# Optimization experiments

Measured on AMD Instinct MI355X. Metric: run time of the kernel, lower is better.

Reference implementation:

```python
import jax, jax.numpy as jnp
import numpy as np

N = 50000      # nodes
E = 800000     # edges (before self-loops)
IN = 512       # in_dim
HID = 128      # hidden_dim
HEADS = 4
NEG_SLOPE = 0.2


def setup_inputs() -> dict:
    key = jax.random.key(0)
    ks = jax.random.split(key, 20)
    s = 0.05
    inp = {
        'x': jax.random.normal(ks[0], (N, IN), jnp.float32),
        'edge_index': jax.random.randint(ks[1], (2, E), 0, N, dtype=jnp.int32),
        # layer 0: GATConv(IN -> HID, heads=HEADS)
        'W0': jax.random.normal(ks[2], (HEADS * HID, IN), jnp.float32) * s,
        'a_src0': jax.random.normal(ks[3], (HEADS, HID), jnp.float32) * s,
        'a_dst0': jax.random.normal(ks[4], (HEADS, HID), jnp.float32) * s,
        'b0': jnp.zeros((HEADS * HID,), jnp.float32),
        # layer 1: GATConv(HEADS*HID -> HID, heads=HEADS)
        'W1': jax.random.normal(ks[5], (HEADS * HID, HEADS * HID), jnp.float32) * s,
        'a_src1': jax.random.normal(ks[6], (HEADS, HID), jnp.float32) * s,
        'a_dst1': jax.random.normal(ks[7], (HEADS, HID), jnp.float32) * s,
        'b1': jnp.zeros((HEADS * HID,), jnp.float32),
        # layer 2: GATConv(HEADS*HID -> HID, heads=1)
        'W2': jax.random.normal(ks[8], (HID, HEADS * HID), jnp.float32) * s,
        'a_src2': jax.random.normal(ks[9], (1, HID), jnp.float32) * s,
        'a_dst2': jax.random.normal(ks[10], (1, HID), jnp.float32) * s,
        'b2': jnp.zeros((HID,), jnp.float32),
        # output heads
        'Wv': jax.random.normal(ks[11], (HID, HID), jnp.float32) * s,
        'bv': jnp.zeros((HID,), jnp.float32),
        'Wt': jax.random.normal(ks[12], (HID, HID), jnp.float32) * s,
        'bt': jnp.zeros((HID,), jnp.float32),
    }
    return inp


def _gat_conv(x, src, dst, W, a_src, a_dst, bias, heads, n_nodes):
    """PyG-style GATConv (eval mode, att_dropout=0, self-loops pre-added)."""
    ch = a_src.shape[-1]
    h = (x @ W.T).reshape(n_nodes, heads, ch)            # [N,H,C]
    alpha_s = jnp.einsum('nhc,hc->nh', h, a_src)          # [N,H]
    alpha_d = jnp.einsum('nhc,hc->nh', h, a_dst)          # [N,H]
    e = alpha_s[src] + alpha_d[dst]                       # [E,H]
    e = jnp.where(e > 0, e, NEG_SLOPE * e)                # leaky_relu(0.2)
    # segment softmax over destination nodes
    m = jax.ops.segment_max(e, dst, num_segments=n_nodes)  # [N,H]
    e = jnp.exp(e - m[dst])
    z = jax.ops.segment_sum(e, dst, num_segments=n_nodes)  # [N,H]
    alpha = e / (z[dst] + 1e-16)                          # [E,H]
    msg = h[src] * alpha[:, :, None]                      # [E,H,C]
    out = jax.ops.segment_sum(msg, dst, num_segments=n_nodes)  # [N,H,C]
    return out.reshape(n_nodes, heads * ch) + bias


def reference(x, edge_index, W0, a_src0, a_dst0, b0, W1, a_src1, a_dst1, b1,
              W2, a_src2, a_dst2, b2, Wv, bv, Wt, bt):
    n = x.shape[0]
    loops = jnp.arange(n, dtype=edge_index.dtype)
    src = jnp.concatenate([edge_index[0], loops])
    dst = jnp.concatenate([edge_index[1], loops])

    h = _gat_conv(x, src, dst, W0, a_src0, a_dst0, b0, HEADS, n)
    h = jax.nn.relu(h)                                    # dropout is no-op in eval
    h = _gat_conv(h, src, dst, W1, a_src1, a_dst1, b1, HEADS, n)
    h = jax.nn.relu(h)
    h = _gat_conv(h, src, dst, W2, a_src2, a_dst2, b2, 1, n)  # [N,HID]

    x_vision = jax.nn.relu(h @ Wv.T + bv)
    x_text = jax.nn.relu(h @ Wt.T + bt)
    return (h, x_vision, x_text)
```

## Files before the change

kernel.cpp:

```cpp
#include <hip/hip_runtime.h>
#include <hip/hip_bf16.h>
#include <math.h>

typedef __bf16 bf16;
typedef __bf16 bf16x2 __attribute__((ext_vector_type(2)));
typedef __bf16 bf16x4 __attribute__((ext_vector_type(4)));
typedef __bf16 bf16x8 __attribute__((ext_vector_type(8)));
typedef float f32x4 __attribute__((ext_vector_type(4)));

#define NNODES 50000
#define NEDGES 800000

static __device__ __forceinline__ void gld_lds16(const void* g, void* l) {
    __builtin_amdgcn_global_load_lds((__attribute__((address_space(1))) void*)g,
                                     (__attribute__((address_space(3))) void*)l,
                                     16, 0, 0);
}

__global__ void detect_kernel(const unsigned int* __restrict__ xw, int* __restrict__ flag)
{
    const int l = threadIdx.x;
    int c = 0;
    for (int i = l; i < 4096; i += 64) {
        const unsigned int b1 = (xw[i] >> 8) & 0x7Fu;
        c += (b1 >= 0x34u && b1 <= 0x43u) ? 1 : 0;
    }
#pragma unroll
    for (int off = 32; off; off >>= 1) c += __shfl_xor(c, off);
    if (l == 0) *flag = (c < 2048) ? 1 : 0;
}

__global__ __launch_bounds__(256) void zero_out_kernel(void* out, long n, const int* __restrict__ flag)
{
    const int fp32 = *flag;
    const long i = (long)blockIdx.x * 256 + threadIdx.x;
    if (i < n) {
        if (fp32) ((float*)out)[i] = 0.f;
        else ((bf16*)out)[i] = (bf16)0.f;
    }
}

__global__ __launch_bounds__(256) void convert4_kernel(
    const void* __restrict__ in, bf16* __restrict__ out, int n4, const int* __restrict__ flag)
{
    const int fp32 = *flag;
    const int i = blockIdx.x * 256 + threadIdx.x;
    if (i >= n4) return;
    bf16x4 o;
    if (fp32) {
        const float4 v = ((const float4*)in)[i];
        o[0] = (bf16)v.x; o[1] = (bf16)v.y; o[2] = (bf16)v.z; o[3] = (bf16)v.w;
    } else {
        o = ((const bf16x4*)in)[i];
    }
    ((bf16x4*)out)[i] = o;
}

struct CvtBatch { const void* in[16]; bf16* out[16]; int n4[16]; };

__global__ __launch_bounds__(256) void convert_batch_kernel(CvtBatch b, const int* __restrict__ flag)
{
    const int fp32 = *flag;
    const int it = blockIdx.y;
    const int n4 = b.n4[it];
    const void* in = b.in[it];
    bf16* out = b.out[it];
    for (int i = blockIdx.x * 256 + threadIdx.x; i < n4; i += gridDim.x * 256) {
        bf16x4 o;
        if (fp32) {
            const float4 v = ((const float4*)in)[i];
            o[0] = (bf16)v.x; o[1] = (bf16)v.y; o[2] = (bf16)v.z; o[3] = (bf16)v.w;
        } else {
            o = ((const bf16x4*)in)[i];
        }
        ((bf16x4*)out)[i] = o;
    }
}

__global__ __launch_bounds__(256) void gemm_bt(
    const bf16* __restrict__ A, const bf16* __restrict__ B,
    bf16* __restrict__ C, int M, int N, int K,
    const bf16* __restrict__ av, const bf16* __restrict__ dv,
    float* __restrict__ aS, float* __restrict__ aD, int H)
{
    __shared__ __align__(16) bf16 As[128 * 32];
    __shared__ __align__(16) bf16 Bs[128 * 32];
    __shared__ float sPS[128];
    __shared__ float sPD[128];
    const int tid  = threadIdx.x;
    const int lane = tid & 63;
    const int w    = tid >> 6;
    const int wm   = (w >> 1) * 64, wn = (w & 1) * 64;
    const int mBase = blockIdx.y * 128, nBase = blockIdx.x * 128;
    const int hb = nBase >> 7;

    f32x4 acc[4][4];
#pragma unroll
    for (int i = 0; i < 4; i++)
#pragma unroll
        for (int j = 0; j < 4; j++)
#pragma unroll
            for (int r = 0; r < 4; r++) acc[i][j][r] = 0.f;

    const int rA   = tid >> 2;
    const int kseg = (tid & 3) * 8;
    int ra0 = mBase + rA;       if (ra0 > M - 1) ra0 = M - 1;
    int ra1 = mBase + rA + 64;  if (ra1 > M - 1) ra1 = M - 1;
    const bf16* gA0 = A + (long)ra0 * K + kseg;
    const bf16* gA1 = A + (long)ra1 * K + kseg;
    const bf16* gB0 = B + (long)(nBase + rA) * K + kseg;
    const bf16* gB1 = B + (long)(nBase + rA + 64) * K + kseg;
    bf16* lA0 = &As[tid * 8];
    bf16* lA1 = &As[(tid + 256) * 8];
    bf16* lB0 = &Bs[tid * 8];
    bf16* lB1 = &Bs[(tid + 256) * 8];

    const int quad = lane >> 4, l16 = lane & 15;

    if (tid < 128) { sPS[tid] = 0.f; sPD[tid] = 0.f; }

    for (int k0 = 0; k0 < K; k0 += 32) {
        gld_lds16(gA0 + k0, lA0);
        gld_lds16(gA1 + k0, lA1);
        gld_lds16(gB0 + k0, lB0);
        gld_lds16(gB1 + k0, lB1);
        __syncthreads();
        bf16x8 af[4], bfr[4];
#pragma unroll
        for (int i = 0; i < 4; i++) {
            af[i]  = *(const bf16x8*)&As[(wm + i * 16 + l16) * 32 + quad * 8];
            bfr[i] = *(const bf16x8*)&Bs[(wn + i * 16 + l16) * 32 + quad * 8];
        }
#pragma unroll
        for (int i = 0; i < 4; i++)
#pragma unroll
            for (int j = 0; j < 4; j++)
                acc[i][j] = __builtin_amdgcn_mfma_f32_16x16x32_bf16(af[i], bfr[j], acc[i][j], 0, 0, 0);
        __syncthreads();
    }

    float aval[4], dval[4];
#pragma unroll
    for (int j = 0; j < 4; j++) {
        const int cg = nBase + wn + j * 16 + l16;
        aval[j] = (float)av[cg];
        dval[j] = (float)dv[cg];
    }
#pragma unroll
    for (int i = 0; i < 4; i++) {
#pragma unroll
        for (int r = 0; r < 4; r++) {
            float ps = 0.f, pd = 0.f;
#pragma unroll
            for (int j = 0; j < 4; j++) {
                ps += acc[i][j][r] * aval[j];
                pd += acc[i][j][r] * dval[j];
            }
#pragma unroll
            for (int off = 8; off; off >>= 1) {
                ps += __shfl_xor(ps, off);
                pd += __shfl_xor(pd, off);
            }
            if (l16 == 0) {
                const int rl = wm + i * 16 + quad * 4 + r;
                atomicAdd(&sPS[rl], ps);
                atomicAdd(&sPD[rl], pd);
            }
        }
    }

#pragma unroll
    for (int i = 0; i < 4; i++) {
        const int row0 = mBase + wm + i * 16 + quad * 4;
#pragma unroll
        for (int j = 0; j < 4; j++) {
            const int colg = nBase + wn + j * 16 + l16;
#pragma unroll
            for (int r = 0; r < 4; r++) {
                const int row = row0 + r;
                if (row < M) C[(long)row * N + colg] = (bf16)acc[i][j][r];
            }
        }
    }

    __syncthreads();
    if (tid < 128) {
        const int row = mBase + tid;
        if (row < M) {
            aS[(long)row * H + hb] = sPS[tid];
            aD[(long)row * H + hb] = sPD[tid];
        }
    }
}

__global__ void hist_kernel(const int* __restrict__ dst, int* __restrict__ cnt, int E)
{
    const int e = blockIdx.x * blockDim.x + threadIdx.x;
    if (e < E) atomicAdd(&cnt[dst[e]], 1);
}

__global__ __launch_bounds__(256) void scan1_kernel(
    const int* __restrict__ cnt, int* __restrict__ rowptr, int* __restrict__ blksum, int n)
{
    __shared__ int buf[256];
    const int b = blockIdx.x, t = threadIdx.x, i = b * 256 + t;
    const int v = (i < n) ? cnt[i] : 0;
    buf[t] = v;
    __syncthreads();
    for (int off = 1; off < 256; off <<= 1) {
        const int add = (t >= off) ? buf[t - off] : 0;
        __syncthreads();
        buf[t] += add;
        __syncthreads();
    }
    if (i < n) rowptr[i + 1] = buf[t];
    if (t == 255) blksum[b] = buf[255];
    if (b == 0 && t == 0) rowptr[0] = 0;
}

__global__ __launch_bounds__(256) void scan2_kernel(int* __restrict__ blksum, int nb)
{
    __shared__ int buf[256];
    const int t = threadIdx.x;
    const int v = (t < nb) ? blksum[t] : 0;
    buf[t] = v;
    __syncthreads();
    for (int off = 1; off < 256; off <<= 1) {
        const int add = (t >= off) ? buf[t - off] : 0;
        __syncthreads();
        buf[t] += add;
        __syncthreads();
    }
    if (t < nb) blksum[t] = buf[t] - v;
}

__global__ __launch_bounds__(256) void scan3_kernel(
    int* __restrict__ rowptr, const int* __restrict__ blksum, int n)
{
    const int b = blockIdx.x, i = b * 256 + threadIdx.x;
    if (i < n) rowptr[i + 1] += blksum[b];
}

__global__ void fill_kernel(const int* __restrict__ src, const int* __restrict__ dst,
                            const int* __restrict__ rowptr, int* __restrict__ off,
                            int* __restrict__ col, int E)
{
    const int e = blockIdx.x * blockDim.x + threadIdx.x;
    if (e < E) {
        const int d = dst[e];
        const int p = rowptr[d] + atomicAdd(&off[d], 1);
        col[p] = src[e];
    }
}

__global__ __launch_bounds__(256) void agg4s_kernel(
    const bf16* __restrict__ h, const float* __restrict__ asrc,
    const float* __restrict__ adst, const int* __restrict__ rowptr,
    const int* __restrict__ col, const bf16* __restrict__ bias,
    bf16* __restrict__ out, int NB)
{
    __shared__ int2 ew_s[4][64];
    const int w = threadIdx.x >> 6, lane = threadIdx.x & 63;
    const int g = lane >> 4, li = lane & 15;
    const int s = blockIdx.x / NB;
    const int n = (blockIdx.x % NB) * 4 + w;
    const float ad = adst[(long)n * 4 + s];
    const int start = rowptr[n];
    const int deg   = rowptr[n + 1] - start;
    const int total = deg + 1;

    float z = 0.f;
    float acc[8];
#pragma unroll
    for (int c = 0; c < 8; c++) acc[c] = 0.f;
    const char* hbp = (const char*)h;
    const int sOff = s * 256 + li * 16;
    const int2* ews = ew_s[w];

    for (int base = 0; base < total; base += 64) {
        const int i = base + lane;
        const bool valid = i < total;
        const int sv = (i < deg) ? col[start + i] : n;
        float e = asrc[(long)sv * 4 + s] + ad;
        e = (e > 0.f) ? e : 0.2f * e;
        e = fminf(fmaxf(e, -60.f), 60.f);
        const float wv = valid ? __expf(e) : 0.f;
        ew_s[w][lane] = make_int2(sv << 10, __float_as_int(wv));
        __builtin_amdgcn_wave_barrier();
        const int cnt = min(64, total - base);
        int j = 0;
        for (; j + 16 <= cnt; j += 16) {
            const int2 v0 = ews[j + g];
            const int2 v1 = ews[j + 4 + g];
            const int2 v2 = ews[j + 8 + g];
            const int2 v3 = ews[j + 12 + g];
            const bf16x8 h0 = *(const bf16x8*)(hbp + (v0.x + sOff));
            const bf16x8 h1 = *(const bf16x8*)(hbp + (v1.x + sOff));
            const bf16x8 h2 = *(const bf16x8*)(hbp + (v2.x + sOff));
            const bf16x8 h3 = *(const bf16x8*)(hbp + (v3.x + sOff));
            const float w0 = __int_as_float(v0.y), w1 = __int_as_float(v1.y);
            const float w2 = __int_as_float(v2.y), w3 = __int_as_float(v3.y);
            z += w0 + w1 + w2 + w3;
#pragma unroll
            for (int c = 0; c < 8; c++) {
                acc[c] += w0 * (float)h0[c];
                acc[c] += w1 * (float)h1[c];
                acc[c] += w2 * (float)h2[c];
                acc[c] += w3 * (float)h3[c];
            }
        }
        for (; j < cnt; j += 4) {
            const int2 v = ews[j + g];
            const float ww = __int_as_float(v.y);
            z += ww;
            const bf16x8 hv = *(const bf16x8*)(hbp + (v.x + sOff));
#pragma unroll
            for (int c = 0; c < 8; c++) acc[c] += ww * (float)hv[c];
        }
        __builtin_amdgcn_wave_barrier();
    }

#pragma unroll
    for (int c = 0; c < 8; c++) {
        acc[c] += __shfl_xor(acc[c], 16);
        acc[c] += __shfl_xor(acc[c], 32);
    }
    z += __shfl_xor(z, 16);
    z += __shfl_xor(z, 32);

    if (g == 0) {
        const float rz = 1.f / (z + 1e-16f);
        const bf16x8 b8 = *(const bf16x8*)(bias + s * 128 + li * 8);
        bf16x8 ov;
#pragma unroll
        for (int c = 0; c < 8; c++)
            ov[c] = (bf16)fmaxf(acc[c] * rz + (float)b8[c], 0.f);
        *(bf16x8*)(out + (long)n * 512 + s * 128 + li * 8) = ov;
    }
}

__global__ __launch_bounds__(256) void agg1g_kernel(
    const bf16* __restrict__ h, const float* __restrict__ asrc,
    const float* __restrict__ adst, const int* __restrict__ rowptr,
    const int* __restrict__ col, const bf16* __restrict__ bias,
    void* __restrict__ outv, const int* __restrict__ dflag)
{
    __shared__ int2 ew_s[4][64];
    const int w = threadIdx.x >> 6, lane = threadIdx.x & 63;
    const int g = lane >> 4, li = lane & 15;
    const int n = blockIdx.x * 4 + w;
    if (n >= NNODES) return;
    const int fp32out = *dflag;
    const float ad = adst[n];
    const int start = rowptr[n];
    const int deg   = rowptr[n + 1] - start;
    const int total = deg + 1;

    float z = 0.f;
    float acc[8];
#pragma unroll
    for (int c = 0; c < 8; c++) acc[c] = 0.f;
    const char* hbp = (const char*)h;
    const int sOff = li * 16;
    const int2* ews = ew_s[w];

    for (int base = 0; base < total; base += 64) {
        const int i = base + lane;
        const bool valid = i < total;
        const int sv = (i < deg) ? col[start + i] : n;
        float e = asrc[sv] + ad;
        e = (e > 0.f) ? e : 0.2f * e;
        e = fminf(fmaxf(e, -60.f), 60.f);
        const float wv = valid ? __expf(e) : 0.f;
        ew_s[w][lane] = make_int2(sv << 8, __float_as_int(wv));
        __builtin_amdgcn_wave_barrier();
        const int cnt = min(64, total - base);
        int j = 0;
        for (; j + 16 <= cnt; j += 16) {
            const int2 v0 = ews[j + g];
            const int2 v1 = ews[j + 4 + g];
            const int2 v2 = ews[j + 8 + g];
            const int2 v3 = ews[j + 12 + g];
            const bf16x8 h0 = *(const bf16x8*)(hbp + (v0.x + sOff));
            const bf16x8 h1 = *(const bf16x8*)(hbp + (v1.x + sOff));
            const bf16x8 h2 = *(const bf16x8*)(hbp + (v2.x + sOff));
            const bf16x8 h3 = *(const bf16x8*)(hbp + (v3.x + sOff));
            const float w0 = __int_as_float(v0.y), w1 = __int_as_float(v1.y);
            const float w2 = __int_as_float(v2.y), w3 = __int_as_float(v3.y);
            z += w0 + w1 + w2 + w3;
#pragma unroll
            for (int c = 0; c < 8; c++) {
                acc[c] += w0 * (float)h0[c];
                acc[c] += w1 * (float)h1[c];
                acc[c] += w2 * (float)h2[c];
                acc[c] += w3 * (float)h3[c];
            }
        }
        for (; j < cnt; j += 4) {
            const int2 v = ews[j + g];
            const float ww = __int_as_float(v.y);
            z += ww;
            const bf16x8 hv = *(const bf16x8*)(hbp + (v.x + sOff));
#pragma unroll
            for (int c = 0; c < 8; c++) acc[c] += ww * (float)hv[c];
        }
        __builtin_amdgcn_wave_barrier();
    }

#pragma unroll
    for (int c = 0; c < 8; c++) {
        acc[c] += __shfl_xor(acc[c], 16);
        acc[c] += __shfl_xor(acc[c], 32);
    }
    z += __shfl_xor(z, 16);
    z += __shfl_xor(z, 32);

    if (g == 0) {
        const float rz = 1.f / (z + 1e-16f);
        float o[8];
#pragma unroll
        for (int c = 0; c < 8; c++)
            o[c] = acc[c] * rz + (float)bias[li * 8 + c];
        if (fp32out) {
            float* op = (float*)outv + (long)n * 128 + li * 8;
            f32x4 o0, o1;
#pragma unroll
            for (int c = 0; c < 4; c++) { o0[c] = o[c]; o1[c] = o[c + 4]; }
            *(f32x4*)op = o0;
            *(f32x4*)(op + 4) = o1;
        } else {
            bf16x8 ov;
#pragma unroll
            for (int c = 0; c < 8; c++) ov[c] = (bf16)o[c];
            *(bf16x8*)((bf16*)outv + (long)n * 128 + li * 8) = ov;
        }
    }
}

__global__ __launch_bounds__(256) void heads_kernel(
    const void* __restrict__ hbase, void* __restrict__ outv,
    const bf16* __restrict__ Wv, const bf16* __restrict__ bv,
    const bf16* __restrict__ Wt, const bf16* __restrict__ bt,
    const int* __restrict__ dflag, int N)
{
    const int fp32 = *dflag;
    __shared__ float hbuf[32][128];
    const int n0 = blockIdx.x * 32, t = threadIdx.x;
    for (int i = t; i < 32 * 128; i += 256) {
        const int node = n0 + (i >> 7), c = i & 127;
        float v = 0.f;
        if (node < N)
            v = fp32 ? ((const float*)hbase)[(long)node * 128 + c]
                     : (float)((const bf16*)hbase)[(long)node * 128 + c];
        hbuf[i >> 7][c] = v;
    }
    __syncthreads();
    const int m = t & 127;
    const bool vis = t < 128;
    const bf16* W = vis ? Wv : Wt;
    const float b = (float)(vis ? bv[m] : bt[m]);
    float acc[32];
#pragma unroll
    for (int i = 0; i < 32; i++) acc[i] = 0.f;
    for (int k0 = 0; k0 < 128; k0 += 8) {
        const bf16x8 wv8 = *(const bf16x8*)&W[m * 128 + k0];
#pragma unroll
        for (int kk = 0; kk < 8; kk++) {
            const float wk = (float)wv8[kk];
#pragma unroll
            for (int i = 0; i < 32; i++) acc[i] += hbuf[i][k0 + kk] * wk;
        }
    }
    const long sec = vis ? (long)N * 128 : (long)2 * N * 128;
#pragma unroll
    for (int i = 0; i < 32; i++) {
        const int node = n0 + i;
        if (node < N) {
            float o = fmaxf(acc[i] + b, 0.f);
            const long idx = sec + (long)node * 128 + m;
            if (fp32) ((float*)outv)[idx] = o;
            else ((bf16*)outv)[idx] = (bf16)o;
        }
    }
}

extern "C" void kernel_launch(void* const* d_in, const int* in_sizes, int n_in,
                              void* d_out, int out_size, void* d_ws, size_t ws_size,
                              hipStream_t stream)
{
    const int N = NNODES, E = NEDGES;
    const int* srcp = (const int*)d_in[1];
    const int* dstp = srcp + E;

    char* p0 = (char*)d_ws;
    char* p = p0;
    auto bump = [&](size_t b) { char* r = p; p += (b + 255) & ~(size_t)255; return r; };
    int*   dflag  = (int*)bump(256);
    bf16*  xc     = (bf16*)bump((size_t)N * 512 * 2);
    bf16*  W0c    = (bf16*)bump(262144 * 2);
    bf16*  as0c   = (bf16*)bump(512 * 2);
    bf16*  ad0c   = (bf16*)bump(512 * 2);
    bf16*  b0c    = (bf16*)bump(512 * 2);
    bf16*  W1c    = (bf16*)bump(262144 * 2);
    bf16*  as1c   = (bf16*)bump(512 * 2);
    bf16*  ad1c   = (bf16*)bump(512 * 2);
    bf16*  b1c    = (bf16*)bump(512 * 2);
    bf16*  W2c    = (bf16*)bump(65536 * 2);
    bf16*  as2c   = (bf16*)bump(128 * 2);
    bf16*  ad2c   = (bf16*)bump(128 * 2);
    bf16*  b2c    = (bf16*)bump(128 * 2);
    bf16*  Wvc    = (bf16*)bump(16384 * 2);
    bf16*  bvc    = (bf16*)bump(128 * 2);
    bf16*  Wtc    = (bf16*)bump(16384 * 2);
    bf16*  btc    = (bf16*)bump(128 * 2);
    int*   cnt    = (int*)bump((size_t)N * 4);
    int*   offs   = (int*)bump((size_t)N * 4);
    int*   rowptr = (int*)bump((size_t)(N + 1) * 4);
    int*   blksum = (int*)bump(256 * 4);
    int*   colarr = (int*)bump((size_t)E * 4);
    float* alphaS = (float*)bump((size_t)N * 4 * 4);
    float* alphaD = (float*)bump((size_t)N * 4 * 4);
    bf16*  bufA   = (bf16*)bump((size_t)N * 512 * 2);
    bf16*  bufB   = (bf16*)bump((size_t)N * 512 * 2);
    const size_t need = (size_t)(p - p0);

    detect_kernel<<<1, 64, 0, stream>>>((const unsigned int*)d_in[0], dflag);

    if (need > ws_size) {
        zero_out_kernel<<<((long)out_size + 255) / 256, 256, 0, stream>>>(d_out, out_size, dflag);
        return;
    }

    convert4_kernel<<<(N * 512 / 4 + 255) / 256, 256, 0, stream>>>(d_in[0], xc, N * 512 / 4, dflag);
    CvtBatch cb;
    const void* ins[16] = {d_in[2], d_in[3], d_in[4], d_in[5], d_in[6], d_in[7], d_in[8], d_in[9],
                           d_in[10], d_in[11], d_in[12], d_in[13], d_in[14], d_in[15], d_in[16], d_in[17]};
    bf16* outs[16] = {W0c, as0c, ad0c, b0c, W1c, as1c, ad1c, b1c,
                      W2c, as2c, ad2c, b2c, Wvc, bvc, Wtc, btc};
    const int ns4[16] = {65536, 128, 128, 128, 65536, 128, 128, 128,
                         16384, 32, 32, 32, 4096, 32, 4096, 32};
    for (int i = 0; i < 16; i++) { cb.in[i] = ins[i]; cb.out[i] = outs[i]; cb.n4[i] = ns4[i]; }
    convert_batch_kernel<<<dim3(64, 16), 256, 0, stream>>>(cb, dflag);

    const int nb = (N + 255) / 256;
    hipMemsetAsync(cnt, 0, (size_t)N * 4, stream);
    hipMemsetAsync(offs, 0, (size_t)N * 4, stream);
    hist_kernel<<<(E + 255) / 256, 256, 0, stream>>>(dstp, cnt, E);
    scan1_kernel<<<nb, 256, 0, stream>>>(cnt, rowptr, blksum, N);
    scan2_kernel<<<1, 256, 0, stream>>>(blksum, nb);
    scan3_kernel<<<nb, 256, 0, stream>>>(rowptr, blksum, N);
    fill_kernel<<<(E + 255) / 256, 256, 0, stream>>>(srcp, dstp, rowptr, offs, colarr, E);

    const int NB = N / 4;

    dim3 g0(4, (N + 127) / 128);
    gemm_bt<<<g0, 256, 0, stream>>>(xc, W0c, bufA, N, 512, 512,
                                    as0c, ad0c, alphaS, alphaD, 4);
    agg4s_kernel<<<NB * 4, 256, 0, stream>>>(bufA, alphaS, alphaD, rowptr, colarr, b0c, bufB, NB);

    gemm_bt<<<g0, 256, 0, stream>>>(bufB, W1c, bufA, N, 512, 512,
                                    as1c, ad1c, alphaS, alphaD, 4);
    agg4s_kernel<<<NB * 4, 256, 0, stream>>>(bufA, alphaS, alphaD, rowptr, colarr, b1c, bufB, NB);

    dim3 g2(1, (N + 127) / 128);
    gemm_bt<<<g2, 256, 0, stream>>>(bufB, W2c, bufA, N, 128, 512,
                                    as2c, ad2c, alphaS, alphaD, 1);
    agg1g_kernel<<<(N + 3) / 4, 256, 0, stream>>>(bufA, alphaS, alphaD, rowptr, colarr, b2c, d_out, dflag);

    heads_kernel<<<(N + 31) / 32, 256, 0, stream>>>(d_out, d_out, Wvc, bvc, Wtc, btc, dflag, N);
}
```

Before: 817.0 us.

## Map aggregation head slices to XCDs and simplify gather loop unrolling

Result: faster. 797.5 us (-2.4%).

```diff
diff --git a/kernel.cpp b/kernel.cpp
--- a/kernel.cpp
+++ b/kernel.cpp
@@ -262,8 +262,10 @@
     __shared__ int2 ew_s[4][64];
     const int w = threadIdx.x >> 6, lane = threadIdx.x & 63;
     const int g = lane >> 4, li = lane & 15;
-    const int s = blockIdx.x / NB;
-    const int n = (blockIdx.x % NB) * 4 + w;
+    const int xcd = blockIdx.x & 7;
+    const int s = xcd >> 1;
+    const int nbi = ((blockIdx.x >> 3) << 1) | (xcd & 1);
+    const int n = nbi * 4 + w;
     const float ad = adst[(long)n * 4 + s];
     const int start = rowptr[n];
     const int deg   = rowptr[n + 1] - start;
@@ -288,28 +290,8 @@
         ew_s[w][lane] = make_int2(sv << 10, __float_as_int(wv));
         __builtin_amdgcn_wave_barrier();
         const int cnt = min(64, total - base);
-        int j = 0;
-        for (; j + 16 <= cnt; j += 16) {
-            const int2 v0 = ews[j + g];
-            const int2 v1 = ews[j + 4 + g];
-            const int2 v2 = ews[j + 8 + g];
-            const int2 v3 = ews[j + 12 + g];
-            const bf16x8 h0 = *(const bf16x8*)(hbp + (v0.x + sOff));
-            const bf16x8 h1 = *(const bf16x8*)(hbp + (v1.x + sOff));
-            const bf16x8 h2 = *(const bf16x8*)(hbp + (v2.x + sOff));
-            const bf16x8 h3 = *(const bf16x8*)(hbp + (v3.x + sOff));
-            const float w0 = __int_as_float(v0.y), w1 = __int_as_float(v1.y);
-            const float w2 = __int_as_float(v2.y), w3 = __int_as_float(v3.y);
-            z += w0 + w1 + w2 + w3;
-#pragma unroll
-            for (int c = 0; c < 8; c++) {
-                acc[c] += w0 * (float)h0[c];
-                acc[c] += w1 * (float)h1[c];
-                acc[c] += w2 * (float)h2[c];
-                acc[c] += w3 * (float)h3[c];
-            }
-        }
-        for (; j < cnt; j += 4) {
+#pragma unroll 2
+        for (int j = 0; j < cnt; j += 4) {
             const int2 v = ews[j + g];
             const float ww = __int_as_float(v.y);
             z += ww;
@@ -375,28 +357,8 @@
         ew_s[w][lane] = make_int2(sv << 8, __float_as_int(wv));
         __builtin_amdgcn_wave_barrier();
         const int cnt = min(64, total - base);
-        int j = 0;
-        for (; j + 16 <= cnt; j += 16) {
-            const int2 v0 = ews[j + g];
-            const int2 v1 = ews[j + 4 + g];
-            const int2 v2 = ews[j + 8 + g];
-            const int2 v3 = ews[j + 12 + g];
-            const bf16x8 h0 = *(const bf16x8*)(hbp + (v0.x + sOff));
-            const bf16x8 h1 = *(const bf16x8*)(hbp + (v1.x + sOff));
-            const bf16x8 h2 = *(const bf16x8*)(hbp + (v2.x + sOff));
-            const bf16x8 h3 = *(const bf16x8*)(hbp + (v3.x + sOff));
-            const float w0 = __int_as_float(v0.y), w1 = __int_as_float(v1.y);
-            const float w2 = __int_as_float(v2.y), w3 = __int_as_float(v3.y);
-            z += w0 + w1 + w2 + w3;
-#pragma unroll
-            for (int c = 0; c < 8; c++) {
-                acc[c] += w0 * (float)h0[c];
-                acc[c] += w1 * (float)h1[c];
-                acc[c] += w2 * (float)h2[c];
-                acc[c] += w3 * (float)h3[c];
-            }
-        }
-        for (; j < cnt; j += 4) {
+#pragma unroll 2
+        for (int j = 0; j < cnt; j += 4) {
             const int2 v = ews[j + g];
             const float ww = __int_as_float(v.y);
             z += ww;
```
